# Performance work log

Measured on AMD Instinct MI355X. Metric: run time of the kernel, lower is better.

## Reference

```python
import jax, jax.numpy as jnp
import numpy as np

EMBED_DIM = 1024
HEAD_DIM = 64


def setup_inputs() -> dict:
    key = jax.random.key(0)
    ks = jax.random.split(key, 7)
    B, S = 4, 2048
    s = 1.0 / np.sqrt(EMBED_DIM)
    h = jax.random.normal(ks[0], (B, S, EMBED_DIM), dtype=jnp.float32)
    Wq = jax.random.normal(ks[1], (EMBED_DIM, HEAD_DIM), dtype=jnp.float32) * s
    bq = jax.random.normal(ks[2], (HEAD_DIM,), dtype=jnp.float32) * 0.01
    Wk = jax.random.normal(ks[3], (EMBED_DIM, HEAD_DIM), dtype=jnp.float32) * s
    bk = jax.random.normal(ks[4], (HEAD_DIM,), dtype=jnp.float32) * 0.01
    Wv = jax.random.normal(ks[5], (EMBED_DIM, HEAD_DIM), dtype=jnp.float32) * s
    bv = jax.random.normal(ks[6], (HEAD_DIM,), dtype=jnp.float32) * 0.01
    return {"h": h, "Wq": Wq, "bq": bq, "Wk": Wk, "bk": bk, "Wv": Wv, "bv": bv}


def reference(h, Wq, bq, Wk, bk, Wv, bv):
    # Linear projections: h [B,S,E] -> q,k [B,S,D]
    q = jnp.einsum("bse,ed->bsd", h, Wq) + bq
    k = jnp.einsum("bse,ed->bsd", h, Wk) + bk
    v = jnp.einsum("bse,ed->bsd", h, Wv) + bv  # computed but UNUSED (faithful to source)
    del v
    scale = 1.0 / jnp.sqrt(jnp.asarray(HEAD_DIM, dtype=q.dtype))
    # scores [B, Sq, Sk]
    scores = jnp.einsum("bqd,bkd->bqk", q, k) * scale
    # NOTE: source uses softmax over dim=1 (query axis), not the key axis
    weights = jax.nn.softmax(scores, axis=1)
    # NOTE: source passes h (not v) as the value tensor
    out = jnp.einsum("bqk,bke->bqe", weights, h)  # [B, Sq, E]
    return out
```

## Files before the change

kernel.cpp:

```cpp
#include <hip/hip_runtime.h>
#include <hip/hip_bf16.h>
#include <math.h>

#define EMBED 1024
#define HDIM  64
#define BATCH 4
#define SEQ   2048

typedef __attribute__((ext_vector_type(8))) short short8;
typedef __attribute__((ext_vector_type(4))) float f32x4;
typedef unsigned int u32;
typedef unsigned short u16;

static __device__ __forceinline__ u16 f2bf(float f) {
    union { float f; u32 u; } v; v.f = f;
    u32 r = v.u + 0x7fffu + ((v.u >> 16) & 1u);
    return (u16)(r >> 16);
}

static __device__ __forceinline__ void gload_lds16(const u16* g, u16* l) {
    __builtin_amdgcn_global_load_lds(
        (const __attribute__((address_space(1))) u32*)g,
        (__attribute__((address_space(3))) u32*)l, 16, 0, 0);
}

__global__ __launch_bounds__(256) void wt_kernel(
    const float* __restrict__ Wq, const float* __restrict__ Wk,
    u16* __restrict__ WqT, u16* __restrict__ WkT)
{
    __shared__ float tile[64][65];
    const float* W = blockIdx.y ? Wk : Wq;
    u16* WT = blockIdx.y ? WkT : WqT;
    int e0 = blockIdx.x * 64;
    int t = threadIdx.x, c = t & 63, r4 = t >> 6;
    for (int r = r4; r < 64; r += 4)
        tile[r][c] = W[(size_t)(e0 + r) * HDIM + c];
    __syncthreads();
    for (int d = r4; d < 64; d += 4)
        WT[(size_t)d * EMBED + e0 + c] = f2bf(tile[c][d]);
}

__global__ __launch_bounds__(256) void proj_kernel(
    const float* __restrict__ h, const u16* __restrict__ WqT, const u16* __restrict__ WkT,
    const float* __restrict__ bq, const float* __restrict__ bk,
    u16* __restrict__ Qbf, u16* __restrict__ Kbf)
{
    __shared__ u16 hs[2][16][72];
    int b = blockIdx.x >> 7, s0 = (blockIdx.x & 127) * 16;
    int t = threadIdx.x, lane = t & 63, w = t >> 6;
    int l15 = lane & 15, quad = lane >> 4;
    int pj = w >> 1, nh = (w & 1) * 32;
    const float* hb = h + ((size_t)b * SEQ + s0) * EMBED;
    const u16* Wp = pj ? WkT : WqT;
    int r = t >> 4, c4 = (t & 15) * 4;

    f32x4 pre = *(const f32x4*)(hb + (size_t)r * EMBED + c4);
    f32x4 acc[2];
    acc[0] = acc[1] = (f32x4){0.f, 0.f, 0.f, 0.f};

    const u16* Wrow0 = Wp + (size_t)(nh + l15) * EMBED;
    const u16* Wrow1 = Wp + (size_t)(nh + 16 + l15) * EMBED;

    for (int it = 0; it < 16; ++it) {
        int ec = it * 64, buf = it & 1;
        uint2 pk;
        pk.x = (u32)f2bf(pre[0]) | ((u32)f2bf(pre[1]) << 16);
        pk.y = (u32)f2bf(pre[2]) | ((u32)f2bf(pre[3]) << 16);
        *(uint2*)&hs[buf][r][c4] = pk;
        __syncthreads();
        if (it + 1 < 16)
            pre = *(const f32x4*)(hb + (size_t)r * EMBED + ec + 64 + c4);
        short8 bf00 = *(const short8*)(Wrow0 + ec + quad * 8);
        short8 bf01 = *(const short8*)(Wrow0 + ec + 32 + quad * 8);
        short8 bf10 = *(const short8*)(Wrow1 + ec + quad * 8);
        short8 bf11 = *(const short8*)(Wrow1 + ec + 32 + quad * 8);
        short8 a0 = *(const short8*)&hs[buf][l15][quad * 8];
        short8 a1 = *(const short8*)&hs[buf][l15][32 + quad * 8];
        acc[0] = __builtin_amdgcn_mfma_f32_16x16x32_bf16(a0, bf00, acc[0], 0, 0, 0);
        acc[0] = __builtin_amdgcn_mfma_f32_16x16x32_bf16(a1, bf01, acc[0], 0, 0, 0);
        acc[1] = __builtin_amdgcn_mfma_f32_16x16x32_bf16(a0, bf10, acc[1], 0, 0, 0);
        acc[1] = __builtin_amdgcn_mfma_f32_16x16x32_bf16(a1, bf11, acc[1], 0, 0, 0);
    }

    const float* bias = pj ? bk : bq;
    float scale = pj ? 1.0f : 0.125f;
    u16* outp = pj ? Kbf : Qbf;
    float bv0 = bias[nh + l15], bv1 = bias[nh + 16 + l15];
#pragma unroll
    for (int rr = 0; rr < 4; rr++) {
        size_t row = (size_t)b * SEQ + s0 + quad * 4 + rr;
        outp[row * HDIM + nh + l15]      = f2bf((acc[0][rr] + bv0) * scale);
        outp[row * HDIM + nh + 16 + l15] = f2bf((acc[1][rr] + bv1) * scale);
    }
}

__global__ __launch_bounds__(256) void stats_kernel(
    const u16* __restrict__ Qbf, const u16* __restrict__ Kbf,
    float* __restrict__ mArr, float* __restrict__ lArr)
{
    __shared__ float sm[4][16], sl[4][16];
    int b = blockIdx.y;
    int k0 = blockIdx.x * 16;
    int t = threadIdx.x, lane = t & 63, w = t >> 6;
    int l15 = lane & 15, quad = lane >> 4;
    const u16* Qb = Qbf + (size_t)b * SEQ * HDIM;
    const u16* Kb = Kbf + (size_t)b * SEQ * HDIM;
    short8 kf0 = *(const short8*)(Kb + (size_t)(k0 + l15) * HDIM + quad * 8);
    short8 kf1 = *(const short8*)(Kb + (size_t)(k0 + l15) * HDIM + 32 + quad * 8);
    float m_run = -1e30f, l_run = 0.f;
    int qs = w * 512;
    for (int q0 = qs; q0 < qs + 512; q0 += 16) {
        short8 qf0 = *(const short8*)(Qb + (size_t)(q0 + l15) * HDIM + quad * 8);
        short8 qf1 = *(const short8*)(Qb + (size_t)(q0 + l15) * HDIM + 32 + quad * 8);
        f32x4 acc = {0.f, 0.f, 0.f, 0.f};
        acc = __builtin_amdgcn_mfma_f32_16x16x32_bf16(qf0, kf0, acc, 0, 0, 0);
        acc = __builtin_amdgcn_mfma_f32_16x16x32_bf16(qf1, kf1, acc, 0, 0, 0);
        float tm = fmaxf(fmaxf(acc[0], acc[1]), fmaxf(acc[2], acc[3]));
        tm = fmaxf(tm, __shfl_xor(tm, 16, 64));
        tm = fmaxf(tm, __shfl_xor(tm, 32, 64));
        float mn = fmaxf(m_run, tm);
        float p = __expf(acc[0] - mn) + __expf(acc[1] - mn)
                + __expf(acc[2] - mn) + __expf(acc[3] - mn);
        p += __shfl_xor(p, 16, 64);
        p += __shfl_xor(p, 32, 64);
        l_run = l_run * __expf(m_run - mn) + p;
        m_run = mn;
    }
    if (quad == 0) { sm[w][l15] = m_run; sl[w][l15] = l_run; }
    __syncthreads();
    if (t < 16) {
        float m = fmaxf(fmaxf(sm[0][t], sm[1][t]), fmaxf(sm[2][t], sm[3][t]));
        float l = sl[0][t] * __expf(sm[0][t] - m) + sl[1][t] * __expf(sm[1][t] - m)
                + sl[2][t] * __expf(sm[2][t] - m) + sl[3][t] * __expf(sm[3][t] - m);
        mArr[b * SEQ + k0 + t] = m;
        lArr[b * SEQ + k0 + t] = l;
    }
}

__global__ __launch_bounds__(256) void transpose_kernel(
    const float* __restrict__ h, const float* __restrict__ lArr, u16* __restrict__ hT)
{
    __shared__ float tile[64][65];
    int b  = blockIdx.z;
    int s0 = blockIdx.x * 64, e0 = blockIdx.y * 64;
    int t = threadIdx.x, c = t & 63, r4 = t >> 6;
    const float* hb = h + (size_t)b * SEQ * EMBED;
    for (int r = r4; r < 64; r += 4)
        tile[r][c] = hb[(size_t)(s0 + r) * EMBED + e0 + c];
    __syncthreads();
    float il = 1.0f / lArr[b * SEQ + s0 + c];
    u16* hTb = hT + (size_t)b * EMBED * SEQ;
    for (int er = r4; er < 64; er += 4)
        hTb[(size_t)(e0 + er) * SEQ + s0 + c] = f2bf(tile[c][er] * il);
}

__global__ __launch_bounds__(256) void weights_kernel(
    const u16* __restrict__ Qbf, const u16* __restrict__ Kbf,
    const float* __restrict__ mArr, u16* __restrict__ Wmat)
{
    int b = blockIdx.z;
    int q0 = blockIdx.x * 64, k0 = blockIdx.y * 64;
    int t = threadIdx.x, lane = t & 63, w = t >> 6;
    int l15 = lane & 15, quad = lane >> 4;
    const u16* Qb = Qbf + (size_t)b * SEQ * HDIM;
    const u16* Kb = Kbf + (size_t)b * SEQ * HDIM;
    int q = q0 + w * 16;
    short8 qf0 = *(const short8*)(Qb + (size_t)(q + l15) * HDIM + quad * 8);
    short8 qf1 = *(const short8*)(Qb + (size_t)(q + l15) * HDIM + 32 + quad * 8);
    u16* Wb = Wmat + (size_t)b * SEQ * SEQ;
#pragma unroll
    for (int kt = 0; kt < 4; kt++) {
        int k = k0 + kt * 16;
        short8 kf0 = *(const short8*)(Kb + (size_t)(k + l15) * HDIM + quad * 8);
        short8 kf1 = *(const short8*)(Kb + (size_t)(k + l15) * HDIM + 32 + quad * 8);
        f32x4 acc = {0.f, 0.f, 0.f, 0.f};
        acc = __builtin_amdgcn_mfma_f32_16x16x32_bf16(qf0, kf0, acc, 0, 0, 0);
        acc = __builtin_amdgcn_mfma_f32_16x16x32_bf16(qf1, kf1, acc, 0, 0, 0);
        float mv = mArr[b * SEQ + k + l15];
#pragma unroll
        for (int r = 0; r < 4; r++) {
            float wv = __expf(acc[r] - mv);
            Wb[(size_t)(q + quad * 4 + r) * SEQ + k + l15] = f2bf(wv);
        }
    }
}

__global__ __launch_bounds__(256) void out_gemm_kernel(
    const u16* __restrict__ Wmat, const u16* __restrict__ hT, float* __restrict__ out)
{
    __shared__ u16 As[128 * 32];
    __shared__ u16 Bs[128 * 32];
    int b = blockIdx.z;
    int q0 = blockIdx.x * 128, e0 = blockIdx.y * 128;
    int t = threadIdx.x, lane = t & 63, w = t >> 6;
    int l15 = lane & 15, quad = lane >> 4;
    const u16* Wb  = Wmat + (size_t)b * SEQ * SEQ;
    const u16* hTb = hT + (size_t)b * EMBED * SEQ;
    int wq = (w & 1) * 64, we = (w >> 1) * 64;

    f32x4 acc[4][4];
#pragma unroll
    for (int qi = 0; qi < 4; qi++)
#pragma unroll
        for (int ei = 0; ei < 4; ei++) acc[qi][ei] = (f32x4){0.f, 0.f, 0.f, 0.f};

    int srow    = (lane >> 2);
    int scol_l  = (lane & 3) * 8;
    int scol_g  = (((lane & 3) ^ ((lane >> 3) & 3)) * 8);
    int sw      = (quad ^ ((l15 >> 1) & 3)) * 8;

    for (int k0 = 0; k0 < SEQ; k0 += 32) {
        __syncthreads();
#pragma unroll
        for (int ld = 0; ld < 2; ld++) {
            int row = w * 32 + ld * 16 + srow;
            gload_lds16(Wb  + (size_t)(q0 + row) * SEQ + k0 + scol_g, As + row * 32 + scol_l);
            gload_lds16(hTb + (size_t)(e0 + row) * SEQ + k0 + scol_g, Bs + row * 32 + scol_l);
        }
        __syncthreads();

        short8 af[4], bfr[4];
#pragma unroll
        for (int i = 0; i < 4; i++) {
            af[i]  = *(const short8*)(As + (wq + i * 16 + l15) * 32 + sw);
            bfr[i] = *(const short8*)(Bs + (we + i * 16 + l15) * 32 + sw);
        }
#pragma unroll
        for (int qi = 0; qi < 4; qi++)
#pragma unroll
            for (int ei = 0; ei < 4; ei++)
                acc[qi][ei] = __builtin_amdgcn_mfma_f32_16x16x32_bf16(
                    af[qi], bfr[ei], acc[qi][ei], 0, 0, 0);
    }

    float* outb = out + (size_t)b * SEQ * EMBED;
#pragma unroll
    for (int qi = 0; qi < 4; qi++)
#pragma unroll
        for (int ei = 0; ei < 4; ei++)
#pragma unroll
            for (int r = 0; r < 4; r++)
                outb[(size_t)(q0 + wq + qi * 16 + quad * 4 + r) * EMBED
                     + e0 + we + ei * 16 + l15] = acc[qi][ei][r];
}

extern "C" void kernel_launch(void* const* d_in, const int* in_sizes, int n_in,
                              void* d_out, int out_size, void* d_ws, size_t ws_size,
                              hipStream_t stream) {
    (void)in_sizes; (void)n_in; (void)out_size; (void)ws_size;
    const float* h  = (const float*)d_in[0];
    const float* Wq = (const float*)d_in[1];
    const float* bq = (const float*)d_in[2];
    const float* Wk = (const float*)d_in[3];
    const float* bk = (const float*)d_in[4];
    float* out = (float*)d_out;

    char* ws = (char*)d_ws;
    u16*   Qbf  = (u16*)(ws);
    u16*   Kbf  = (u16*)(ws + (1ull << 20));
    u16*   hT   = (u16*)(ws + (2ull << 20));
    float* mArr = (float*)(ws + (18ull << 20));
    float* lArr = (float*)(ws + (18ull << 20) + (64ull << 10));
    u16*   WqT  = (u16*)(ws + (18ull << 20) + (128ull << 10));
    u16*   WkT  = (u16*)(ws + (18ull << 20) + (256ull << 10));
    u16*   Wmat = (u16*)(ws + (19ull << 20));

    hipLaunchKernelGGL(wt_kernel, dim3(16, 2), dim3(256), 0, stream, Wq, Wk, WqT, WkT);
    hipLaunchKernelGGL(proj_kernel, dim3(512), dim3(256), 0, stream,
                       h, WqT, WkT, bq, bk, Qbf, Kbf);
    hipLaunchKernelGGL(stats_kernel, dim3(128, 4), dim3(256), 0, stream,
                       Qbf, Kbf, mArr, lArr);
    hipLaunchKernelGGL(transpose_kernel, dim3(32, 16, 4), dim3(256), 0, stream,
                       h, lArr, hT);
    hipLaunchKernelGGL(weights_kernel, dim3(32, 32, 4), dim3(256), 0, stream,
                       Qbf, Kbf, mArr, Wmat);
    hipLaunchKernelGGL(out_gemm_kernel, dim3(16, 8, 4), dim3(256), 0, stream,
                       Wmat, hT, out);
}
```

Baseline: 214.4 us.

## Fuse h transpose into projection, move 1/l into weights, double-buffer out GEMM

The projection kernel now writes the bf16 transposed h tile from its shared staging buffer, so the separate transpose kernel and its second full read of h are gone. Because hT is produced before the softmax statistics exist, the 1/l normalisation moves into weights_kernel and is applied when each weight is written. The output GEMM gets a double-buffered LDS pipeline with K-tile 64 and an XOR swizzle, issuing the next tile's loads before the current MFMAs to overlap memory with compute. In exchange the proj kernel does extra strided 8-byte global stores, and the larger LDS footprint (64 KB per block) may cut occupancy.

```diff
diff --git a/kernel.cpp b/kernel.cpp
--- a/kernel.cpp
+++ b/kernel.cpp
@@ -43,7 +43,7 @@
 __global__ __launch_bounds__(256) void proj_kernel(
     const float* __restrict__ h, const u16* __restrict__ WqT, const u16* __restrict__ WkT,
     const float* __restrict__ bq, const float* __restrict__ bk,
-    u16* __restrict__ Qbf, u16* __restrict__ Kbf)
+    u16* __restrict__ Qbf, u16* __restrict__ Kbf, u16* __restrict__ hT)
 {
     __shared__ u16 hs[2][16][72];
     int b = blockIdx.x >> 7, s0 = (blockIdx.x & 127) * 16;
@@ -51,8 +51,10 @@
     int l15 = lane & 15, quad = lane >> 4;
     int pj = w >> 1, nh = (w & 1) * 32;
     const float* hb = h + ((size_t)b * SEQ + s0) * EMBED;
+    u16* hTb = hT + (size_t)b * EMBED * SEQ;
     const u16* Wp = pj ? WkT : WqT;
     int r = t >> 4, c4 = (t & 15) * 4;
+    int ej = t >> 2, soff = (t & 3) * 4;
 
     f32x4 pre = *(const f32x4*)(hb + (size_t)r * EMBED + c4);
     f32x4 acc[2];
@@ -70,6 +72,18 @@
         __syncthreads();
         if (it + 1 < 16)
             pre = *(const f32x4*)(hb + (size_t)r * EMBED + ec + 64 + c4);
+
+        {
+            u16 v0 = hs[buf][soff    ][ej];
+            u16 v1 = hs[buf][soff + 1][ej];
+            u16 v2 = hs[buf][soff + 2][ej];
+            u16 v3 = hs[buf][soff + 3][ej];
+            uint2 pk2;
+            pk2.x = (u32)v0 | ((u32)v1 << 16);
+            pk2.y = (u32)v2 | ((u32)v3 << 16);
+            *(uint2*)(hTb + (size_t)(ec + ej) * SEQ + s0 + soff) = pk2;
+        }
+
         short8 bf00 = *(const short8*)(Wrow0 + ec + quad * 8);
         short8 bf01 = *(const short8*)(Wrow0 + ec + 32 + quad * 8);
         short8 bf10 = *(const short8*)(Wrow1 + ec + quad * 8);
@@ -137,26 +151,10 @@
     }
 }
 
-__global__ __launch_bounds__(256) void transpose_kernel(
-    const float* __restrict__ h, const float* __restrict__ lArr, u16* __restrict__ hT)
-{
-    __shared__ float tile[64][65];
-    int b  = blockIdx.z;
-    int s0 = blockIdx.x * 64, e0 = blockIdx.y * 64;
-    int t = threadIdx.x, c = t & 63, r4 = t >> 6;
-    const float* hb = h + (size_t)b * SEQ * EMBED;
-    for (int r = r4; r < 64; r += 4)
-        tile[r][c] = hb[(size_t)(s0 + r) * EMBED + e0 + c];
-    __syncthreads();
-    float il = 1.0f / lArr[b * SEQ + s0 + c];
-    u16* hTb = hT + (size_t)b * EMBED * SEQ;
-    for (int er = r4; er < 64; er += 4)
-        hTb[(size_t)(e0 + er) * SEQ + s0 + c] = f2bf(tile[c][er] * il);
-}
-
 __global__ __launch_bounds__(256) void weights_kernel(
     const u16* __restrict__ Qbf, const u16* __restrict__ Kbf,
-    const float* __restrict__ mArr, u16* __restrict__ Wmat)
+    const float* __restrict__ mArr, const float* __restrict__ lArr,
+    u16* __restrict__ Wmat)
 {
     int b = blockIdx.z;
     int q0 = blockIdx.x * 64, k0 = blockIdx.y * 64;
@@ -176,10 +174,11 @@
         f32x4 acc = {0.f, 0.f, 0.f, 0.f};
         acc = __builtin_amdgcn_mfma_f32_16x16x32_bf16(qf0, kf0, acc, 0, 0, 0);
         acc = __builtin_amdgcn_mfma_f32_16x16x32_bf16(qf1, kf1, acc, 0, 0, 0);
-        float mv = mArr[b * SEQ + k + l15];
+        float mv  = mArr[b * SEQ + k + l15];
+        float inv = 1.0f / lArr[b * SEQ + k + l15];
 #pragma unroll
         for (int r = 0; r < 4; r++) {
-            float wv = __expf(acc[r] - mv);
+            float wv = __expf(acc[r] - mv) * inv;
             Wb[(size_t)(q + quad * 4 + r) * SEQ + k + l15] = f2bf(wv);
         }
     }
@@ -188,8 +187,8 @@
 __global__ __launch_bounds__(256) void out_gemm_kernel(
     const u16* __restrict__ Wmat, const u16* __restrict__ hT, float* __restrict__ out)
 {
-    __shared__ u16 As[128 * 32];
-    __shared__ u16 Bs[128 * 32];
+    __shared__ u16 As[2][128 * 64];
+    __shared__ u16 Bs[2][128 * 64];
     int b = blockIdx.z;
     int q0 = blockIdx.x * 128, e0 = blockIdx.y * 128;
     int t = threadIdx.x, lane = t & 63, w = t >> 6;
@@ -204,34 +203,53 @@
 #pragma unroll
         for (int ei = 0; ei < 4; ei++) acc[qi][ei] = (f32x4){0.f, 0.f, 0.f, 0.f};
 
-    int srow    = (lane >> 2);
-    int scol_l  = (lane & 3) * 8;
-    int scol_g  = (((lane & 3) ^ ((lane >> 3) & 3)) * 8);
-    int sw      = (quad ^ ((l15 >> 1) & 3)) * 8;
-
-    for (int k0 = 0; k0 < SEQ; k0 += 32) {
+    int st_rl = lane >> 3;
+    int st_pc = lane & 7;
+
+#define STAGE(bi, k0)                                                          \
+    {                                                                          \
+        _Pragma("unroll")                                                      \
+        for (int ld = 0; ld < 4; ld++) {                                       \
+            int rowb = w * 32 + ld * 8;                                        \
+            int row  = rowb + st_rl;                                           \
+            int cg   = st_pc ^ (row & 7);            \
+            gload_lds16(Wb  + (size_t)(q0 + row) * SEQ + (k0) + cg * 8,        \
+                        &As[bi][rowb * 64] + lane * 8);                        \
+            gload_lds16(hTb + (size_t)(e0 + row) * SEQ + (k0) + cg * 8,        \
+                        &Bs[bi][rowb * 64] + lane * 8);                        \
+        }                                                                      \
+    }
+
+    STAGE(0, 0)
+
+    for (int it = 0; it < 32; ++it) {
+        int buf = it & 1;
         __syncthreads();
-#pragma unroll
-        for (int ld = 0; ld < 2; ld++) {
-            int row = w * 32 + ld * 16 + srow;
-            gload_lds16(Wb  + (size_t)(q0 + row) * SEQ + k0 + scol_g, As + row * 32 + scol_l);
-            gload_lds16(hTb + (size_t)(e0 + row) * SEQ + k0 + scol_g, Bs + row * 32 + scol_l);
-        }
-        __syncthreads();
-
-        short8 af[4], bfr[4];
-#pragma unroll
-        for (int i = 0; i < 4; i++) {
-            af[i]  = *(const short8*)(As + (wq + i * 16 + l15) * 32 + sw);
-            bfr[i] = *(const short8*)(Bs + (we + i * 16 + l15) * 32 + sw);
-        }
+        if (it + 1 < 32) STAGE(buf ^ 1, (it + 1) * 64)
+
+        short8 af[2][4], bfr[2][4];
+#pragma unroll
+        for (int kf = 0; kf < 2; kf++)
+#pragma unroll
+            for (int i = 0; i < 4; i++) {
+                int ra = wq + i * 16 + l15;
+                int rb = we + i * 16 + l15;
+                int pca = (kf * 4 + quad) ^ (ra & 7);
+                int pcb = (kf * 4 + quad) ^ (rb & 7);
+                af[kf][i]  = *(const short8*)(&As[buf][ra * 64] + pca * 8);
+                bfr[kf][i] = *(const short8*)(&Bs[buf][rb * 64] + pcb * 8);
+            }
 #pragma unroll
         for (int qi = 0; qi < 4; qi++)
 #pragma unroll
-            for (int ei = 0; ei < 4; ei++)
+            for (int ei = 0; ei < 4; ei++) {
                 acc[qi][ei] = __builtin_amdgcn_mfma_f32_16x16x32_bf16(
-                    af[qi], bfr[ei], acc[qi][ei], 0, 0, 0);
-    }
+                    af[0][qi], bfr[0][ei], acc[qi][ei], 0, 0, 0);
+                acc[qi][ei] = __builtin_amdgcn_mfma_f32_16x16x32_bf16(
+                    af[1][qi], bfr[1][ei], acc[qi][ei], 0, 0, 0);
+            }
+    }
+#undef STAGE
 
     float* outb = out + (size_t)b * SEQ * EMBED;
 #pragma unroll
@@ -267,13 +285,11 @@
 
     hipLaunchKernelGGL(wt_kernel, dim3(16, 2), dim3(256), 0, stream, Wq, Wk, WqT, WkT);
     hipLaunchKernelGGL(proj_kernel, dim3(512), dim3(256), 0, stream,
-                       h, WqT, WkT, bq, bk, Qbf, Kbf);
+                       h, WqT, WkT, bq, bk, Qbf, Kbf, hT);
     hipLaunchKernelGGL(stats_kernel, dim3(128, 4), dim3(256), 0, stream,
                        Qbf, Kbf, mArr, lArr);
-    hipLaunchKernelGGL(transpose_kernel, dim3(32, 16, 4), dim3(256), 0, stream,
-                       h, lArr, hT);
     hipLaunchKernelGGL(weights_kernel, dim3(32, 32, 4), dim3(256), 0, stream,
-                       Qbf, Kbf, mArr, Wmat);
+                       Qbf, Kbf, mArr, lArr, Wmat);
     hipLaunchKernelGGL(out_gemm_kernel, dim3(16, 8, 4), dim3(256), 0, stream,
                        Wmat, hT, out);
 }
```

After: 216.9 us. About the same (+1.2%).
